# Optimization experiments

Hardware: AMD Instinct MI355X
Metric: run time of the kernel (lower is better)

Reference implementation:

```python
import jax, jax.numpy as jnp
import numpy as np

B, N, D = 4, 1024, 1024
H, DH = 16, 64
N_LAYERS = 3  # len(mlp_dims) - 1 with implicit_mlp_hiddens=(64, 64)
EPS = 1.1920929e-07  # torch.nn.RMSNorm default eps = finfo(float32).eps


def _rope_tables(n, dtype):
    # lucidrains RotaryEmbedding: theta=10000, interleaved freq repeat
    inv_freq = 1.0 / (10000.0 ** (np.arange(0, DH, 2, dtype=np.float64) / DH))
    t = np.arange(n, dtype=np.float64)[:, None] * inv_freq[None, :]  # [n, DH/2]
    t = np.repeat(t, 2, axis=-1)  # [n, DH], freqs interleaved (f0,f0,f1,f1,...)
    return jnp.asarray(np.cos(t), dtype), jnp.asarray(np.sin(t), dtype)


def _rope_rotate(x, cos, sin):
    # x: [b,h,n,d]; rotate_half on interleaved pairs: (x1,x2) -> (-x2,x1)
    xp = x.reshape(*x.shape[:-1], DH // 2, 2)
    xr = jnp.stack((-xp[..., 1], xp[..., 0]), axis=-1).reshape(x.shape)
    return x * cos + xr * sin


def _attend(q, k, v):
    # rotate_queries_with_cached_keys with no cache: same positions for q and k
    n = q.shape[-2]
    cos, sin = _rope_tables(n, q.dtype)
    q = _rope_rotate(q, cos, sin)
    k = _rope_rotate(k, cos, sin)
    scale = DH ** -0.5
    scores = jnp.einsum('bhqd,bhkd->bhqk', q, k) * scale
    causal = jnp.tril(jnp.ones((n, n), dtype=bool))
    scores = jnp.where(causal, scores, -jnp.inf)
    attn = jax.nn.softmax(scores, axis=-1)
    return jnp.einsum('bhqk,bhkd->bhqd', attn, v)


def _split_heads(x):
    b, n, _ = x.shape
    return x.reshape(b, n, H, DH).transpose(0, 2, 1, 3)  # b h n d


def setup_inputs() -> dict:
    key = jax.random.key(0)
    ks = jax.random.split(key, 6)
    s = 0.02
    return {
        'tokens': jax.random.normal(ks[0], (B, N, D), jnp.float32),
        'gamma': jnp.ones((D,), jnp.float32),                                  # RMSNorm weight
        'Wq': jax.random.normal(ks[1], (D, H * DH), jnp.float32) * s,           # to_queries
        'Wk': jax.random.normal(ks[2], (N_LAYERS, D, H * DH), jnp.float32) * s, # stacked key projections
        'Wv': jax.random.normal(ks[3], (N_LAYERS, D, H * DH), jnp.float32) * s, # stacked value projections
        'Wo': jax.random.normal(ks[4], (H * DH, D), jnp.float32) * s,           # to_out
    }


def reference(tokens, gamma, Wq, Wk, Wv, Wo):
    b, n, d = tokens.shape
    # RMSNorm (prenorm)
    x = tokens * jax.lax.rsqrt(jnp.mean(tokens * tokens, axis=-1, keepdims=True) + EPS) * gamma
    out = _split_heads(x @ Wq)  # queries, [b h n d]
    for i in range(N_LAYERS):
        k = _split_heads(x @ Wk[i])
        v = _split_heads(x @ Wv[i])
        out = _attend(out, k, v)
        if i < N_LAYERS - 1:
            out = jax.nn.silu(out)  # implicit MLP activation between attention stages
    out = out.transpose(0, 2, 1, 3).reshape(b, n, H * DH)  # merge heads
    return out @ Wo
```

## Files before the change

### kernel.cpp

```cpp
#include <hip/hip_runtime.h>


typedef unsigned short u16;
typedef short s16x8 __attribute__((ext_vector_type(8)));
typedef u16 u16x4 __attribute__((ext_vector_type(4)));
typedef float f32x4 __attribute__((ext_vector_type(4)));

typedef __attribute__((address_space(1))) const unsigned int as1c_uint;
typedef __attribute__((address_space(3))) unsigned int as3_uint;

__device__ __forceinline__ float b2f(u16 h) {
  union { unsigned int u; float f; } v; v.u = ((unsigned int)h) << 16; return v.f;
}
__device__ __forceinline__ u16 f2b(float f) {
  union { float f; unsigned int u; } v; v.f = f;
  return (u16)((v.u + 0x7FFFu + ((v.u >> 16) & 1u)) >> 16);
}
__device__ __forceinline__ void gload16(const u16* g, const u16* lds) {
  __builtin_amdgcn_global_load_lds((as1c_uint*)(size_t)g,
                                   (as3_uint*)(unsigned int)(size_t)lds, 16, 0, 0);
}

__global__ __launch_bounds__(256)
void rmsnorm_kernel(const float* __restrict__ T, const float* __restrict__ gamma,
                    u16* __restrict__ X) {
  const int row = blockIdx.x, tid = threadIdx.x;
  const float4 v = ((const float4*)(T + (size_t)row * 1024))[tid];
  float ss = v.x * v.x + v.y * v.y + v.z * v.z + v.w * v.w;
#pragma unroll
  for (int msk = 1; msk <= 32; msk <<= 1) ss += __shfl_xor(ss, msk, 64);
  __shared__ float red[4];
  if ((tid & 63) == 0) red[tid >> 6] = ss;
  __syncthreads();
  const float tot = red[0] + red[1] + red[2] + red[3];
  const float r = rsqrtf(tot * (1.0f / 1024.0f) + 1.1920929e-07f);
  const float4 gm = ((const float4*)gamma)[tid];
  u16x4 o;
  o[0] = f2b(v.x * r * gm.x); o[1] = f2b(v.y * r * gm.y);
  o[2] = f2b(v.z * r * gm.z); o[3] = f2b(v.w * r * gm.w);
  *(u16x4*)(X + (size_t)row * 1024 + tid * 4) = o;
}

__global__ __launch_bounds__(256)
void rope_kernel(float* __restrict__ ct, float* __restrict__ st) {
  const int idx = blockIdx.x * 256 + threadIdx.x;
  const int n = idx >> 5, j = idx & 31;
  const double freq = pow(10000.0, -(double)j / 32.0);
  const double a = (double)n * freq;
  ct[idx] = (float)cos(a);
  st[idx] = (float)sin(a);
}

__global__ __launch_bounds__(256)
void transw_kernel(const float* __restrict__ Wq, const float* __restrict__ Wk,
                   const float* __restrict__ Wv, const float* __restrict__ Wo,
                   u16* __restrict__ wt) {
  __shared__ float tile[64][65];
  const int z = blockIdx.z;
  const float* src = (z == 0) ? Wq
                   : (z <= 3) ? (Wk + (size_t)(z - 1) * 1048576)
                   : (z <= 6) ? (Wv + (size_t)(z - 4) * 1048576)
                              : Wo;
  u16* dst = wt + (size_t)z * 1048576;
  const int tid = threadIdx.x;
  const int bx = blockIdx.x * 64;
  const int by = blockIdx.y * 64;
  const int tcol = (tid & 15) * 4, trow = tid >> 4;
#pragma unroll
  for (int i = 0; i < 4; ++i) {
    const int r = trow + i * 16;
    const float4 v = *(const float4*)(src + (size_t)(bx + r) * 1024 + by + tcol);
    tile[r][tcol] = v.x; tile[r][tcol + 1] = v.y;
    tile[r][tcol + 2] = v.z; tile[r][tcol + 3] = v.w;
  }
  __syncthreads();
  const int k4 = (tid & 15) * 4;
#pragma unroll
  for (int j = 0; j < 4; ++j) {
    const int R = (tid >> 4) + j * 16;
    u16x4 o;
    o[0] = f2b(tile[k4][R]);     o[1] = f2b(tile[k4 + 1][R]);
    o[2] = f2b(tile[k4 + 2][R]); o[3] = f2b(tile[k4 + 3][R]);
    *(u16x4*)&dst[(size_t)(by + R) * 1024 + bx + k4] = o;
  }
}

template <int KIND>
__global__ __launch_bounds__(256, 2)
void gemm_kernel(const u16* __restrict__ A, const u16* __restrict__ Bt,
                 void* __restrict__ Cout, const float* __restrict__ ct,
                 const float* __restrict__ st) {
  constexpr int MB = (KIND == 0) ? 8 : 4;
  constexpr int BM = MB * 32;
  constexpr int ASLOT = BM * 32;
  constexpr int SLOT = (BM + 128) * 32;
  const int p = blockIdx.x;
  const int role = (p & 7) * (KIND == 0 ? 112 : 64) + (p >> 3);
  const int z = (KIND == 0) ? (role >> 7) : (role >> 8);
  const int rem = (KIND == 0) ? (role & 127) : (role & 255);
  const int m0 = (rem >> 3) * BM;
  const int n0 = (rem & 7) * 128;

  const int tid = threadIdx.x;
  const int w = tid >> 6, l = tid & 63;
  const int g = l >> 4, ll = l & 15;
  const int wr = w >> 1, wc = w & 1;

  const u16* Ab;
  const u16* Bb;
  if (KIND == 0) {
    Ab = A + (size_t)m0 * 1024;
    Bb = Bt + (size_t)z * 1048576 + (size_t)n0 * 1024;
  } else {
    Ab = A + (size_t)m0 * 1024 + z * 512;
    Bb = Bt + (size_t)n0 * 1024 + z * 512;
  }

  __shared__ u16 SH[3][SLOT];

  const f32x4 zero = {0.f, 0.f, 0.f, 0.f};
  f32x4 acc[MB][4];
#pragma unroll
  for (int i = 0; i < MB; ++i)
#pragma unroll
    for (int j = 0; j < 4; ++j) acc[i][j] = zero;

  auto stage = [&](int t2) {
    const int slot = t2 % 3;
    const int k0 = t2 * 32;
    const int rsub = l >> 2, sl = l & 3;
#pragma unroll
    for (int c = 0; c < MB / 2; ++c) {
      const int chunk = c * 4 + w;
      const int row = chunk * 16 + rsub;
      const int kk = k0 + ((sl ^ ((row >> 1) & 3)) << 3);
      gload16(Ab + (size_t)row * 1024 + kk, &SH[slot][chunk * 512]);
    }
#pragma unroll
    for (int c = 0; c < 2; ++c) {
      const int chunk = c * 4 + w;
      const int row = chunk * 16 + rsub;
      const int kk = k0 + ((sl ^ ((row >> 1) & 3)) << 3);
      gload16(Bb + (size_t)row * 1024 + kk, &SH[slot][ASLOT + chunk * 512]);
    }
  };

  const int NT = (KIND == 1) ? 16 : 32;
  stage(0); stage(1);

#pragma unroll
  for (int t = 0; t < NT; ++t) {
    if (t < NT - 1) {
      if constexpr (KIND == 0) asm volatile("s_waitcnt vmcnt(6)" ::: "memory");
      else                     asm volatile("s_waitcnt vmcnt(4)" ::: "memory");
    } else {
      asm volatile("s_waitcnt vmcnt(0)" ::: "memory");
    }
    __builtin_amdgcn_s_barrier();

    const int slot = t % 3;
    const u16* As = &SH[slot][0];
    const u16* Bs = &SH[slot][ASLOT];
    s16x8 bfr[4];
#pragma unroll
    for (int nf = 0; nf < 4; ++nf) {
      const int row = wc * 64 + nf * 16 + ll;
      bfr[nf] = *(const s16x8*)&Bs[row * 32 + ((g ^ ((row >> 1) & 3)) << 3)];
    }
    s16x8 af[MB];
#pragma unroll
    for (int mf = 0; mf < MB; ++mf) {
      const int row = wr * (MB * 16) + mf * 16 + ll;
      af[mf] = *(const s16x8*)&As[row * 32 + ((g ^ ((row >> 1) & 3)) << 3)];
    }

    if (t + 2 < NT) stage(t + 2);

    __builtin_amdgcn_s_setprio(1);
#pragma unroll
    for (int mf = 0; mf < MB; ++mf)
#pragma unroll
      for (int nf = 0; nf < 4; ++nf)
        acc[mf][nf] = __builtin_amdgcn_mfma_f32_16x16x32_bf16(af[mf], bfr[nf],
                                                              acc[mf][nf], 0, 0, 0);
    __builtin_amdgcn_s_setprio(0);
  }
  __syncthreads();

  if (KIND == 0) {
    u16* C = (u16*)Cout + (size_t)z * 4194304;
    if (z < 4) {
      const bool doRope = (z >= 1);
      u16* T = &SH[0][0];
#pragma unroll
      for (int mf = 0; mf < MB; ++mf)
#pragma unroll
        for (int nf = 0; nf < 4; ++nf) {
          const int c = wc * 64 + nf * 16 + ll;
#pragma unroll
          for (int rg = 0; rg < 4; ++rg) {
            const int r = wr * (MB * 16) + mf * 16 + g * 4 + rg;
            T[r * 128 + (c ^ ((r & 7) << 4))] = f2b(acc[mf][nf][rg]);
          }
        }
      __syncthreads();
#pragma unroll
      for (int i = 0; i < BM / 16; ++i) {
        const int R = (tid >> 4) + i * 16;
        const int c0 = (tid & 15) * 8;
        s16x8 v = *(const s16x8*)&T[R * 128 + (c0 ^ ((R & 7) << 4))];
        if (doRope) {
          const int n = (m0 + R) & 1023;
          const int j0 = (c0 & 63) >> 1;
          const float4 c4 = *(const float4*)(ct + n * 32 + j0);
          const float4 s4 = *(const float4*)(st + n * 32 + j0);
          s16x8 vo;
#pragma unroll
          for (int pp = 0; pp < 4; ++pp) {
            const float c = ((const float*)&c4)[pp];
            const float s = ((const float*)&s4)[pp];
            const float x0 = b2f((u16)v[2 * pp]), x1 = b2f((u16)v[2 * pp + 1]);
            vo[2 * pp]     = (short)f2b(x0 * c - x1 * s);
            vo[2 * pp + 1] = (short)f2b(x1 * c + x0 * s);
          }
          v = vo;
        }
        *(s16x8*)&C[(size_t)(m0 + R) * 1024 + n0 + c0] = v;
      }
    } else {
#pragma unroll
      for (int mf = 0; mf < MB; ++mf)
#pragma unroll
        for (int nf = 0; nf < 4; ++nf) {
          const int col = n0 + wc * 64 + nf * 16 + ll;
          const int hh = col >> 6, d = col & 63;
          const int mb = m0 + wr * (MB * 16) + mf * 16 + g * 4;
          const int bb = mb >> 10, n = mb & 1023;
          u16x4 pk;
#pragma unroll
          for (int rg = 0; rg < 4; ++rg) pk[rg] = f2b(acc[mf][nf][rg]);
          *(u16x4*)&C[((size_t)((bb * 16 + hh) * 64 + d)) * 1024 + n] = pk;
        }
    }
  } else {
    float* C = (float*)Cout + (size_t)z * 4194304;
#pragma unroll
    for (int mf = 0; mf < MB; ++mf)
#pragma unroll
      for (int nf = 0; nf < 4; ++nf) {
        const int col = n0 + wc * 64 + nf * 16 + ll;
#pragma unroll
        for (int rg = 0; rg < 4; ++rg) {
          const int m = m0 + wr * (MB * 16) + mf * 16 + g * 4 + rg;
          C[(size_t)m * 1024 + col] = acc[mf][nf][rg];
        }
      }
  }
}

__global__ __launch_bounds__(256)
void reduce_kernel(const float* __restrict__ P, float* __restrict__ out) {
  const int i = (blockIdx.x * 256 + threadIdx.x) * 4;
  const float4 a = *(const float4*)(P + i);
  const float4 b = *(const float4*)(P + 4194304 + i);
  float4 o;
  o.x = a.x + b.x; o.y = a.y + b.y; o.z = a.z + b.z; o.w = a.w + b.w;
  *(float4*)(out + i) = o;
}

template <int SILU>
__global__ __launch_bounds__(256)
void attn_kernel(const u16* __restrict__ Q, const u16* __restrict__ K,
                 const u16* __restrict__ Vt, u16* __restrict__ O,
                 const float* __restrict__ ct, const float* __restrict__ st) {
  const int lin = blockIdx.x + (blockIdx.y << 3);
  const int role = (lin & 7) * 64 + (lin >> 3);
  const int p = role & 7, bh = role >> 3;
  const int q_lo = p, q_hi = 15 - p;
  const int b = bh >> 4, h = bh & 15;
  const int tid = threadIdx.x, w = tid >> 6, l = tid & 63;
  const int g = l >> 4, ll = l & 15;

  const u16* Qb = Q + (size_t)(b * 1024) * 1024 + h * 64;
  const u16* Kb = K + (size_t)(b * 1024) * 1024 + h * 64;
  const u16* Vb = Vt + (size_t)((b * 16 + h) * 64) * 1024;
  u16* Ob = O + (size_t)(b * 1024) * 1024 + h * 64;

  __shared__ u16 Ksh[2][128 * 72];
  __shared__ u16 Psh[4][16 * 72];

  s16x8 qfL[2], qfH[2];
  auto loadQ = [&](int qt, s16x8* qf) {
    const int qrow = qt * 64 + w * 16 + ll;
#pragma unroll
    for (int kc = 0; kc < 2; ++kc) {
      const int d0 = kc * 32 + g * 8;
      const int j0 = d0 >> 1;
      const float4 c4 = *(const float4*)(ct + qrow * 32 + j0);
      const float4 s4v = *(const float4*)(st + qrow * 32 + j0);
      const s16x8 qin = *(const s16x8*)(Qb + (size_t)qrow * 1024 + d0);
      s16x8 qo;
#pragma unroll
      for (int pp = 0; pp < 4; ++pp) {
        const float c = ((const float*)&c4)[pp], s = ((const float*)&s4v)[pp];
        const float x0 = b2f((u16)qin[2 * pp]), x1 = b2f((u16)qin[2 * pp + 1]);
        qo[2 * pp]     = (short)f2b((x0 * c - x1 * s) * 0.125f);
        qo[2 * pp + 1] = (short)f2b((x1 * c + x0 * s) * 0.125f);
      }
      qf[kc] = qo;
    }
  };
  loadQ(q_lo, qfL);
  loadQ(q_hi, qfH);

  float lsL[4], lsH[4];
  f32x4 oL[4], oH[4];
  const f32x4 zero = {0.f, 0.f, 0.f, 0.f};
#pragma unroll
  for (int rg = 0; rg < 4; ++rg) { lsL[rg] = 0.f; lsH[rg] = 0.f; }
#pragma unroll
  for (int df = 0; df < 4; ++df) { oL[df] = zero; oH[df] = zero; }

  const int srow = tid >> 2;
  const int sc0 = (tid & 3) * 16;

  s16x8 kr0, kr1, kr2, kr3;
  auto kload = [&](int tt) {
    const u16* kp = Kb + (size_t)(tt * 128 + srow) * 1024 + sc0;
    kr0 = *(const s16x8*)kp;
    kr1 = *(const s16x8*)(kp + 8);
    const u16* kp2 = kp + (size_t)64 * 1024;
    kr2 = *(const s16x8*)kp2;
    kr3 = *(const s16x8*)(kp2 + 8);
  };
  auto kstore = [&](int bf) {
    *(s16x8*)&Ksh[bf][srow * 72 + sc0] = kr0;
    *(s16x8*)&Ksh[bf][srow * 72 + sc0 + 8] = kr1;
    *(s16x8*)&Ksh[bf][(64 + srow) * 72 + sc0] = kr2;
    *(s16x8*)&Ksh[bf][(64 + srow) * 72 + sc0 + 8] = kr3;
  };

  kload(0);
  kstore(0);
  __syncthreads();
  int buf = 0;

  const int iters = (q_hi + 2) >> 1;
  for (int tt = 0; tt < iters; ++tt) {
    const bool pre = (tt + 1 < iters);
    if (pre) kload(tt + 1);

    s16x8 vb[2][2][4];
#pragma unroll
    for (int sub = 0; sub < 2; ++sub)
#pragma unroll
      for (int kc = 0; kc < 2; ++kc)
#pragma unroll
        for (int df = 0; df < 4; ++df)
          vb[sub][kc][df] = *(const s16x8*)(Vb + (size_t)(df * 16 + ll) * 1024 +
                                           (tt * 2 + sub) * 64 + kc * 32 + g * 8);

    auto process = [&](const s16x8* qf, float* ls, f32x4* o, int sub,
                       bool diag) {
      const int rb = sub * 64;
      f32x4 s4[4];
      __builtin_amdgcn_s_setprio(1);
#pragma unroll
      for (int nf = 0; nf < 4; ++nf) {
        const s16x8 kb0 = *(const s16x8*)&Ksh[buf][(rb + nf * 16 + ll) * 72 + g * 8];
        const s16x8 kb1 = *(const s16x8*)&Ksh[buf][(rb + nf * 16 + ll) * 72 + 32 + g * 8];
        f32x4 sv = zero;
        sv = __builtin_amdgcn_mfma_f32_16x16x32_bf16(qf[0], kb0, sv, 0, 0, 0);
        sv = __builtin_amdgcn_mfma_f32_16x16x32_bf16(qf[1], kb1, sv, 0, 0, 0);
        s4[nf] = sv;
      }
      __builtin_amdgcn_s_setprio(0);

      if (diag) {
#pragma unroll
        for (int nf = 0; nf < 4; ++nf)
#pragma unroll
          for (int rg = 0; rg < 4; ++rg)
            if (nf * 16 + ll > w * 16 + g * 4 + rg) s4[nf][rg] = -3.0e38f;
      }

#pragma unroll
      for (int rg = 0; rg < 4; ++rg) {
        float ps = 0.f;
#pragma unroll
        for (int nf = 0; nf < 4; ++nf) {
          const float pv = __expf(s4[nf][rg] - 12.f);
          s4[nf][rg] = pv;
          ps += pv;
        }
        ls[rg] += ps;
      }

#pragma unroll
      for (int nf = 0; nf < 4; ++nf)
#pragma unroll
        for (int rg = 0; rg < 4; ++rg)
          Psh[w][(g * 4 + rg) * 72 + nf * 16 + ll] = f2b(s4[nf][rg]);

      __builtin_amdgcn_s_setprio(1);
#pragma unroll
      for (int kc = 0; kc < 2; ++kc) {
        const s16x8 pa = *(const s16x8*)&Psh[w][ll * 72 + kc * 32 + g * 8];
#pragma unroll
        for (int df = 0; df < 4; ++df)
          o[df] = __builtin_amdgcn_mfma_f32_16x16x32_bf16(pa, vb[sub][kc][df],
                                                          o[df], 0, 0, 0);
      }
      __builtin_amdgcn_s_setprio(0);
    };

    const int ka = 2 * tt, kb = 2 * tt + 1;
    process(qfH, lsH, oH, 0, ka == q_hi);
    if (kb <= q_hi) process(qfH, lsH, oH, 1, kb == q_hi);
    if (ka <= q_lo) process(qfL, lsL, oL, 0, ka == q_lo);
    if (kb <= q_lo) process(qfL, lsL, oL, 1, kb == q_lo);

    if (pre) kstore(buf ^ 1);
    __syncthreads();
    buf ^= 1;
  }

  auto finish = [&](float* ls, f32x4* o, int qt) {
#pragma unroll
    for (int rg = 0; rg < 4; ++rg) {
      float v = ls[rg];
      v += __shfl_xor(v, 1, 64);
      v += __shfl_xor(v, 2, 64);
      v += __shfl_xor(v, 4, 64);
      v += __shfl_xor(v, 8, 64);
      ls[rg] = 1.f / v;
    }
#pragma unroll
    for (int df = 0; df < 4; ++df)
#pragma unroll
      for (int rg = 0; rg < 4; ++rg) {
        float val = o[df][rg] * ls[rg];
        if (SILU) val = val / (1.f + __expf(-val));
        Ob[(size_t)(qt * 64 + w * 16 + g * 4 + rg) * 1024 + df * 16 + ll] =
            f2b(val);
      }
  };
  finish(lsH, oH, q_hi);
  finish(lsL, oL, q_lo);
}

extern "C" void kernel_launch(void* const* d_in, const int* in_sizes, int n_in,
                              void* d_out, int out_size, void* d_ws, size_t ws_size,
                              hipStream_t stream) {
  (void)in_sizes; (void)n_in; (void)out_size; (void)ws_size;
  const float* tokens = (const float*)d_in[0];
  const float* gamma  = (const float*)d_in[1];
  const float* Wq     = (const float*)d_in[2];
  const float* Wk     = (const float*)d_in[3];
  const float* Wv     = (const float*)d_in[4];
  const float* Wo     = (const float*)d_in[5];
  float* out = (float*)d_out;

  u16* x    = (u16*)d_ws;
  u16* wt   = x + (size_t)4096 * 1024;
  u16* qkv  = wt + (size_t)8 * 1048576;
  u16* outA = qkv + (size_t)7 * 4194304;
  u16* outB = outA + 4194304;
  float* ct = (float*)(outB + 4194304);
  float* st = ct + 32768;
  float* Pp = (float*)(qkv + 1 * 4194304);

  rmsnorm_kernel<<<4096, 256, 0, stream>>>(tokens, gamma, x);
  rope_kernel<<<128, 256, 0, stream>>>(ct, st);
  transw_kernel<<<dim3(16, 16, 8), 256, 0, stream>>>(Wq, Wk, Wv, Wo, wt);
  gemm_kernel<0><<<896, 256, 0, stream>>>(x, wt, qkv, ct, st);

  const size_t M4 = 4194304;
  attn_kernel<1><<<dim3(8, 64), 256, 0, stream>>>(qkv, qkv + 1 * M4, qkv + 4 * M4,
                                                  outA, ct, st);
  attn_kernel<1><<<dim3(8, 64), 256, 0, stream>>>(outA, qkv + 2 * M4, qkv + 5 * M4,
                                                  outB, ct, st);
  attn_kernel<0><<<dim3(8, 64), 256, 0, stream>>>(outB, qkv + 3 * M4, qkv + 6 * M4,
                                                  outA, ct, st);

  gemm_kernel<1><<<512, 256, 0, stream>>>(outA, wt + (size_t)7 * 1048576,
                                          (void*)Pp, ct, st);
  reduce_kernel<<<4096, 256, 0, stream>>>(Pp, out);
}
```

Measured before the change: 228.8 us.

## Load K fragments directly from global memory instead of staging through LDS

Removes the double-buffered shared-memory K tile and the per-iteration block barrier. Each wave now loads its own K MFMA fragments straight from global memory per 64-key tile, and the loop steps one 64-key tile at a time instead of two. This drops LDS traffic and __syncthreads, but all four waves now fetch the same K data redundantly through cache and lose the register prefetch overlap.

```diff
diff --git a/kernel.cpp b/kernel.cpp
--- a/kernel.cpp
+++ b/kernel.cpp
@@ -286,7 +286,6 @@
   const u16* Vb = Vt + (size_t)((b * 16 + h) * 64) * 1024;
   u16* Ob = O + (size_t)(b * 1024) * 1024 + h * 64;
 
-  __shared__ u16 Ksh[2][128 * 72];
   __shared__ u16 Psh[4][16 * 72];
 
   s16x8 qfL[2], qfH[2];
@@ -321,57 +320,30 @@
 #pragma unroll
   for (int df = 0; df < 4; ++df) { oL[df] = zero; oH[df] = zero; }
 
-  const int srow = tid >> 2;
-  const int sc0 = (tid & 3) * 16;
-
-  s16x8 kr0, kr1, kr2, kr3;
-  auto kload = [&](int tt) {
-    const u16* kp = Kb + (size_t)(tt * 128 + srow) * 1024 + sc0;
-    kr0 = *(const s16x8*)kp;
-    kr1 = *(const s16x8*)(kp + 8);
-    const u16* kp2 = kp + (size_t)64 * 1024;
-    kr2 = *(const s16x8*)kp2;
-    kr3 = *(const s16x8*)(kp2 + 8);
-  };
-  auto kstore = [&](int bf) {
-    *(s16x8*)&Ksh[bf][srow * 72 + sc0] = kr0;
-    *(s16x8*)&Ksh[bf][srow * 72 + sc0 + 8] = kr1;
-    *(s16x8*)&Ksh[bf][(64 + srow) * 72 + sc0] = kr2;
-    *(s16x8*)&Ksh[bf][(64 + srow) * 72 + sc0 + 8] = kr3;
-  };
-
-  kload(0);
-  kstore(0);
-  __syncthreads();
-  int buf = 0;
-
-  const int iters = (q_hi + 2) >> 1;
-  for (int tt = 0; tt < iters; ++tt) {
-    const bool pre = (tt + 1 < iters);
-    if (pre) kload(tt + 1);
-
-    s16x8 vb[2][2][4];
-#pragma unroll
-    for (int sub = 0; sub < 2; ++sub)
-#pragma unroll
-      for (int kc = 0; kc < 2; ++kc)
-#pragma unroll
-        for (int df = 0; df < 4; ++df)
-          vb[sub][kc][df] = *(const s16x8*)(Vb + (size_t)(df * 16 + ll) * 1024 +
-                                           (tt * 2 + sub) * 64 + kc * 32 + g * 8);
-
-    auto process = [&](const s16x8* qf, float* ls, f32x4* o, int sub,
-                       bool diag) {
-      const int rb = sub * 64;
+  for (int t = 0; t <= q_hi; ++t) {
+    s16x8 kf[4][2];
+#pragma unroll
+    for (int nf = 0; nf < 4; ++nf) {
+      const u16* kp = Kb + (size_t)(t * 64 + nf * 16 + ll) * 1024 + g * 8;
+      kf[nf][0] = *(const s16x8*)kp;
+      kf[nf][1] = *(const s16x8*)(kp + 32);
+    }
+    s16x8 vb[2][4];
+#pragma unroll
+    for (int kc = 0; kc < 2; ++kc)
+#pragma unroll
+      for (int df = 0; df < 4; ++df)
+        vb[kc][df] = *(const s16x8*)(Vb + (size_t)(df * 16 + ll) * 1024 +
+                                     t * 64 + kc * 32 + g * 8);
+
+    auto process = [&](const s16x8* qf, float* ls, f32x4* o, bool diag) {
       f32x4 s4[4];
       __builtin_amdgcn_s_setprio(1);
 #pragma unroll
       for (int nf = 0; nf < 4; ++nf) {
-        const s16x8 kb0 = *(const s16x8*)&Ksh[buf][(rb + nf * 16 + ll) * 72 + g * 8];
-        const s16x8 kb1 = *(const s16x8*)&Ksh[buf][(rb + nf * 16 + ll) * 72 + 32 + g * 8];
         f32x4 sv = zero;
-        sv = __builtin_amdgcn_mfma_f32_16x16x32_bf16(qf[0], kb0, sv, 0, 0, 0);
-        sv = __builtin_amdgcn_mfma_f32_16x16x32_bf16(qf[1], kb1, sv, 0, 0, 0);
+        sv = __builtin_amdgcn_mfma_f32_16x16x32_bf16(qf[0], kf[nf][0], sv, 0, 0, 0);
+        sv = __builtin_amdgcn_mfma_f32_16x16x32_bf16(qf[1], kf[nf][1], sv, 0, 0, 0);
         s4[nf] = sv;
       }
       __builtin_amdgcn_s_setprio(0);
@@ -408,21 +380,14 @@
         const s16x8 pa = *(const s16x8*)&Psh[w][ll * 72 + kc * 32 + g * 8];
 #pragma unroll
         for (int df = 0; df < 4; ++df)
-          o[df] = __builtin_amdgcn_mfma_f32_16x16x32_bf16(pa, vb[sub][kc][df],
+          o[df] = __builtin_amdgcn_mfma_f32_16x16x32_bf16(pa, vb[kc][df],
                                                           o[df], 0, 0, 0);
       }
       __builtin_amdgcn_s_setprio(0);
     };
 
-    const int ka = 2 * tt, kb = 2 * tt + 1;
-    process(qfH, lsH, oH, 0, ka == q_hi);
-    if (kb <= q_hi) process(qfH, lsH, oH, 1, kb == q_hi);
-    if (ka <= q_lo) process(qfL, lsL, oL, 0, ka == q_lo);
-    if (kb <= q_lo) process(qfL, lsL, oL, 1, kb == q_lo);
-
-    if (pre) kstore(buf ^ 1);
-    __syncthreads();
-    buf ^= 1;
+    process(qfH, lsH, oH, t == q_hi);
+    if (t <= q_lo) process(qfL, lsL, oL, t == q_lo);
   }
 
   auto finish = [&](float* ls, f32x4* o, int qt) {
```

Result: slower. 301.3 us (+31.7%).

## Fuse three chained attention stages into one kernel keeping queries on-chip

Applied to the files above, without the earlier changes.

Merges the three attention launches into a single kernel that loops over the three layers. Each block keeps its output in registers, applies SiLU and RoPE through shared memory, and reuses the result as the next layer's queries. This removes two kernel launches and the global round trips for the intermediate outputs. The trade-off is more register pressure and an extra barrier per layer. Correctness depends on each block's query tiles only needing its own previous outputs, which holds because the same block handles the same rows in every layer.

```diff
diff --git a/kernel.cpp b/kernel.cpp
--- a/kernel.cpp
+++ b/kernel.cpp
@@ -268,11 +268,10 @@
   *(float4*)(out + i) = o;
 }
 
-template <int SILU>
 __global__ __launch_bounds__(256)
-void attn_kernel(const u16* __restrict__ Q, const u16* __restrict__ K,
-                 const u16* __restrict__ Vt, u16* __restrict__ O,
-                 const float* __restrict__ ct, const float* __restrict__ st) {
+void attn_fused_kernel(const u16* __restrict__ qkv, u16* __restrict__ O,
+                       const float* __restrict__ ct, const float* __restrict__ st) {
+  const size_t M4 = 4194304;
   const int lin = blockIdx.x + (blockIdx.y << 3);
   const int role = (lin & 7) * 64 + (lin >> 3);
   const int p = role & 7, bh = role >> 3;
@@ -281,9 +280,7 @@
   const int tid = threadIdx.x, w = tid >> 6, l = tid & 63;
   const int g = l >> 4, ll = l & 15;
 
-  const u16* Qb = Q + (size_t)(b * 1024) * 1024 + h * 64;
-  const u16* Kb = K + (size_t)(b * 1024) * 1024 + h * 64;
-  const u16* Vb = Vt + (size_t)((b * 16 + h) * 64) * 1024;
+  const u16* Qb = qkv + (size_t)(b * 1024) * 1024 + h * 64;
   u16* Ob = O + (size_t)(b * 1024) * 1024 + h * 64;
 
   __shared__ u16 Ksh[2][128 * 72];
@@ -313,140 +310,188 @@
   loadQ(q_lo, qfL);
   loadQ(q_hi, qfH);
 
+  const f32x4 zero = {0.f, 0.f, 0.f, 0.f};
   float lsL[4], lsH[4];
   f32x4 oL[4], oH[4];
-  const f32x4 zero = {0.f, 0.f, 0.f, 0.f};
-#pragma unroll
-  for (int rg = 0; rg < 4; ++rg) { lsL[rg] = 0.f; lsH[rg] = 0.f; }
-#pragma unroll
-  for (int df = 0; df < 4; ++df) { oL[df] = zero; oH[df] = zero; }
 
   const int srow = tid >> 2;
   const int sc0 = (tid & 3) * 16;
 
-  s16x8 kr0, kr1, kr2, kr3;
-  auto kload = [&](int tt) {
-    const u16* kp = Kb + (size_t)(tt * 128 + srow) * 1024 + sc0;
-    kr0 = *(const s16x8*)kp;
-    kr1 = *(const s16x8*)(kp + 8);
-    const u16* kp2 = kp + (size_t)64 * 1024;
-    kr2 = *(const s16x8*)kp2;
-    kr3 = *(const s16x8*)(kp2 + 8);
-  };
-  auto kstore = [&](int bf) {
-    *(s16x8*)&Ksh[bf][srow * 72 + sc0] = kr0;
-    *(s16x8*)&Ksh[bf][srow * 72 + sc0 + 8] = kr1;
-    *(s16x8*)&Ksh[bf][(64 + srow) * 72 + sc0] = kr2;
-    *(s16x8*)&Ksh[bf][(64 + srow) * 72 + sc0 + 8] = kr3;
-  };
-
-  kload(0);
-  kstore(0);
-  __syncthreads();
-  int buf = 0;
-
-  const int iters = (q_hi + 2) >> 1;
-  for (int tt = 0; tt < iters; ++tt) {
-    const bool pre = (tt + 1 < iters);
-    if (pre) kload(tt + 1);
-
-    s16x8 vb[2][2][4];
-#pragma unroll
-    for (int sub = 0; sub < 2; ++sub)
-#pragma unroll
-      for (int kc = 0; kc < 2; ++kc)
+  for (int layer = 0; layer < 3; ++layer) {
+    const u16* Kb = qkv + (size_t)(1 + layer) * M4 + (size_t)(b * 1024) * 1024 + h * 64;
+    const u16* Vb = qkv + (size_t)(4 + layer) * M4 + (size_t)((b * 16 + h) * 64) * 1024;
+
+#pragma unroll
+    for (int rg = 0; rg < 4; ++rg) { lsL[rg] = 0.f; lsH[rg] = 0.f; }
+#pragma unroll
+    for (int df = 0; df < 4; ++df) { oL[df] = zero; oH[df] = zero; }
+
+    s16x8 kr0, kr1, kr2, kr3;
+    auto kload = [&](int tt) {
+      const u16* kp = Kb + (size_t)(tt * 128 + srow) * 1024 + sc0;
+      kr0 = *(const s16x8*)kp;
+      kr1 = *(const s16x8*)(kp + 8);
+      const u16* kp2 = kp + (size_t)64 * 1024;
+      kr2 = *(const s16x8*)kp2;
+      kr3 = *(const s16x8*)(kp2 + 8);
+    };
+    auto kstore = [&](int bf) {
+      *(s16x8*)&Ksh[bf][srow * 72 + sc0] = kr0;
+      *(s16x8*)&Ksh[bf][srow * 72 + sc0 + 8] = kr1;
+      *(s16x8*)&Ksh[bf][(64 + srow) * 72 + sc0] = kr2;
+      *(s16x8*)&Ksh[bf][(64 + srow) * 72 + sc0 + 8] = kr3;
+    };
+
+    kload(0);
+    kstore(0);
+    __syncthreads();
+    int buf = 0;
+
+    const int iters = (q_hi + 2) >> 1;
+    for (int tt = 0; tt < iters; ++tt) {
+      const bool pre = (tt + 1 < iters);
+      if (pre) kload(tt + 1);
+
+      s16x8 vb[2][2][4];
+#pragma unroll
+      for (int sub = 0; sub < 2; ++sub)
+#pragma unroll
+        for (int kc = 0; kc < 2; ++kc)
+#pragma unroll
+          for (int df = 0; df < 4; ++df)
+            vb[sub][kc][df] = *(const s16x8*)(Vb + (size_t)(df * 16 + ll) * 1024 +
+                                             (tt * 2 + sub) * 64 + kc * 32 + g * 8);
+
+      auto process = [&](const s16x8* qf, float* ls, f32x4* o, int sub,
+                         bool diag) {
+        const int rb = sub * 64;
+        f32x4 s4[4];
+        __builtin_amdgcn_s_setprio(1);
+#pragma unroll
+        for (int nf = 0; nf < 4; ++nf) {
+          const s16x8 kb0 = *(const s16x8*)&Ksh[buf][(rb + nf * 16 + ll) * 72 + g * 8];
+          const s16x8 kb1 = *(const s16x8*)&Ksh[buf][(rb + nf * 16 + ll) * 72 + 32 + g * 8];
+          f32x4 sv = zero;
+          sv = __builtin_amdgcn_mfma_f32_16x16x32_bf16(qf[0], kb0, sv, 0, 0, 0);
+          sv = __builtin_amdgcn_mfma_f32_16x16x32_bf16(qf[1], kb1, sv, 0, 0, 0);
+          s4[nf] = sv;
+        }
+        __builtin_amdgcn_s_setprio(0);
+
+        if (diag) {
+#pragma unroll
+          for (int nf = 0; nf < 4; ++nf)
+#pragma unroll
+            for (int rg = 0; rg < 4; ++rg)
+              if (nf * 16 + ll > w * 16 + g * 4 + rg) s4[nf][rg] = -3.0e38f;
+        }
+
+#pragma unroll
+        for (int rg = 0; rg < 4; ++rg) {
+          float ps = 0.f;
+#pragma unroll
+          for (int nf = 0; nf < 4; ++nf) {
+            const float pv = __expf(s4[nf][rg] - 12.f);
+            s4[nf][rg] = pv;
+            ps += pv;
+          }
+          ls[rg] += ps;
+        }
+
+#pragma unroll
+        for (int nf = 0; nf < 4; ++nf)
+#pragma unroll
+          for (int rg = 0; rg < 4; ++rg)
+            Psh[w][(g * 4 + rg) * 72 + nf * 16 + ll] = f2b(s4[nf][rg]);
+
+        __builtin_amdgcn_s_setprio(1);
+#pragma unroll
+        for (int kc = 0; kc < 2; ++kc) {
+          const s16x8 pa = *(const s16x8*)&Psh[w][ll * 72 + kc * 32 + g * 8];
+#pragma unroll
+          for (int df = 0; df < 4; ++df)
+            o[df] = __builtin_amdgcn_mfma_f32_16x16x32_bf16(pa, vb[sub][kc][df],
+                                                            o[df], 0, 0, 0);
+        }
+        __builtin_amdgcn_s_setprio(0);
+      };
+
+      const int ka = 2 * tt, kb2 = 2 * tt + 1;
+      process(qfH, lsH, oH, 0, ka == q_hi);
+      if (kb2 <= q_hi) process(qfH, lsH, oH, 1, kb2 == q_hi);
+      if (ka <= q_lo) process(qfL, lsL, oL, 0, ka == q_lo);
+      if (kb2 <= q_lo) process(qfL, lsL, oL, 1, kb2 == q_lo);
+
+      if (pre) kstore(buf ^ 1);
+      __syncthreads();
+      buf ^= 1;
+    }
+
+    if (layer < 2) {
+      auto toQ = [&](float* ls, f32x4* o, int qt, s16x8* qf) {
+#pragma unroll
+        for (int rg = 0; rg < 4; ++rg) {
+          float v = ls[rg];
+          v += __shfl_xor(v, 1, 64);
+          v += __shfl_xor(v, 2, 64);
+          v += __shfl_xor(v, 4, 64);
+          v += __shfl_xor(v, 8, 64);
+          ls[rg] = 1.f / v;
+        }
 #pragma unroll
         for (int df = 0; df < 4; ++df)
-          vb[sub][kc][df] = *(const s16x8*)(Vb + (size_t)(df * 16 + ll) * 1024 +
-                                           (tt * 2 + sub) * 64 + kc * 32 + g * 8);
-
-    auto process = [&](const s16x8* qf, float* ls, f32x4* o, int sub,
-                       bool diag) {
-      const int rb = sub * 64;
-      f32x4 s4[4];
-      __builtin_amdgcn_s_setprio(1);
-#pragma unroll
-      for (int nf = 0; nf < 4; ++nf) {
-        const s16x8 kb0 = *(const s16x8*)&Ksh[buf][(rb + nf * 16 + ll) * 72 + g * 8];
-        const s16x8 kb1 = *(const s16x8*)&Ksh[buf][(rb + nf * 16 + ll) * 72 + 32 + g * 8];
-        f32x4 sv = zero;
-        sv = __builtin_amdgcn_mfma_f32_16x16x32_bf16(qf[0], kb0, sv, 0, 0, 0);
-        sv = __builtin_amdgcn_mfma_f32_16x16x32_bf16(qf[1], kb1, sv, 0, 0, 0);
-        s4[nf] = sv;
-      }
-      __builtin_amdgcn_s_setprio(0);
-
-      if (diag) {
-#pragma unroll
-        for (int nf = 0; nf < 4; ++nf)
-#pragma unroll
-          for (int rg = 0; rg < 4; ++rg)
-            if (nf * 16 + ll > w * 16 + g * 4 + rg) s4[nf][rg] = -3.0e38f;
-      }
-
-#pragma unroll
-      for (int rg = 0; rg < 4; ++rg) {
-        float ps = 0.f;
-#pragma unroll
-        for (int nf = 0; nf < 4; ++nf) {
-          const float pv = __expf(s4[nf][rg] - 12.f);
-          s4[nf][rg] = pv;
-          ps += pv;
-        }
-        ls[rg] += ps;
-      }
-
-#pragma unroll
-      for (int nf = 0; nf < 4; ++nf)
-#pragma unroll
-        for (int rg = 0; rg < 4; ++rg)
-          Psh[w][(g * 4 + rg) * 72 + nf * 16 + ll] = f2b(s4[nf][rg]);
-
-      __builtin_amdgcn_s_setprio(1);
-#pragma unroll
-      for (int kc = 0; kc < 2; ++kc) {
-        const s16x8 pa = *(const s16x8*)&Psh[w][ll * 72 + kc * 32 + g * 8];
+#pragma unroll
+          for (int rg = 0; rg < 4; ++rg) {
+            float val = o[df][rg] * ls[rg];
+            val = val / (1.f + __expf(-val));
+            Psh[w][(g * 4 + rg) * 72 + df * 16 + ll] = f2b(val);
+          }
+        const int qrow = qt * 64 + w * 16 + ll;
+#pragma unroll
+        for (int kc = 0; kc < 2; ++kc) {
+          const int d0 = kc * 32 + g * 8;
+          const int j0 = d0 >> 1;
+          const float4 c4 = *(const float4*)(ct + qrow * 32 + j0);
+          const float4 s4v = *(const float4*)(st + qrow * 32 + j0);
+          const s16x8 qin = *(const s16x8*)&Psh[w][ll * 72 + d0];
+          s16x8 qo;
+#pragma unroll
+          for (int pp = 0; pp < 4; ++pp) {
+            const float c = ((const float*)&c4)[pp], s = ((const float*)&s4v)[pp];
+            const float x0 = b2f((u16)qin[2 * pp]), x1 = b2f((u16)qin[2 * pp + 1]);
+            qo[2 * pp]     = (short)f2b((x0 * c - x1 * s) * 0.125f);
+            qo[2 * pp + 1] = (short)f2b((x1 * c + x0 * s) * 0.125f);
+          }
+          qf[kc] = qo;
+        }
+      };
+      toQ(lsH, oH, q_hi, qfH);
+      toQ(lsL, oL, q_lo, qfL);
+      __syncthreads();
+    } else {
+      auto finish = [&](float* ls, f32x4* o, int qt) {
+#pragma unroll
+        for (int rg = 0; rg < 4; ++rg) {
+          float v = ls[rg];
+          v += __shfl_xor(v, 1, 64);
+          v += __shfl_xor(v, 2, 64);
+          v += __shfl_xor(v, 4, 64);
+          v += __shfl_xor(v, 8, 64);
+          ls[rg] = 1.f / v;
+        }
 #pragma unroll
         for (int df = 0; df < 4; ++df)
-          o[df] = __builtin_amdgcn_mfma_f32_16x16x32_bf16(pa, vb[sub][kc][df],
-                                                          o[df], 0, 0, 0);
-      }
-      __builtin_amdgcn_s_setprio(0);
-    };
-
-    const int ka = 2 * tt, kb = 2 * tt + 1;
-    process(qfH, lsH, oH, 0, ka == q_hi);
-    if (kb <= q_hi) process(qfH, lsH, oH, 1, kb == q_hi);
-    if (ka <= q_lo) process(qfL, lsL, oL, 0, ka == q_lo);
-    if (kb <= q_lo) process(qfL, lsL, oL, 1, kb == q_lo);
-
-    if (pre) kstore(buf ^ 1);
-    __syncthreads();
-    buf ^= 1;
+#pragma unroll
+          for (int rg = 0; rg < 4; ++rg) {
+            const float val = o[df][rg] * ls[rg];
+            Ob[(size_t)(qt * 64 + w * 16 + g * 4 + rg) * 1024 + df * 16 + ll] =
+                f2b(val);
+          }
+      };
+      finish(lsH, oH, q_hi);
+      finish(lsL, oL, q_lo);
+    }
   }
-
-  auto finish = [&](float* ls, f32x4* o, int qt) {
-#pragma unroll
-    for (int rg = 0; rg < 4; ++rg) {
-      float v = ls[rg];
-      v += __shfl_xor(v, 1, 64);
-      v += __shfl_xor(v, 2, 64);
-      v += __shfl_xor(v, 4, 64);
-      v += __shfl_xor(v, 8, 64);
-      ls[rg] = 1.f / v;
-    }
-#pragma unroll
-    for (int df = 0; df < 4; ++df)
-#pragma unroll
-      for (int rg = 0; rg < 4; ++rg) {
-        float val = o[df][rg] * ls[rg];
-        if (SILU) val = val / (1.f + __expf(-val));
-        Ob[(size_t)(qt * 64 + w * 16 + g * 4 + rg) * 1024 + df * 16 + ll] =
-            f2b(val);
-      }
-  };
-  finish(lsH, oH, q_hi);
-  finish(lsL, oL, q_lo);
 }
 
 extern "C" void kernel_launch(void* const* d_in, const int* in_sizes, int n_in,
@@ -475,13 +520,7 @@
   transw_kernel<<<dim3(16, 16, 8), 256, 0, stream>>>(Wq, Wk, Wv, Wo, wt);
   gemm_kernel<0><<<896, 256, 0, stream>>>(x, wt, qkv, ct, st);
 
-  const size_t M4 = 4194304;
-  attn_kernel<1><<<dim3(8, 64), 256, 0, stream>>>(qkv, qkv + 1 * M4, qkv + 4 * M4,
-                                                  outA, ct, st);
-  attn_kernel<1><<<dim3(8, 64), 256, 0, stream>>>(outA, qkv + 2 * M4, qkv + 5 * M4,
-                                                  outB, ct, st);
-  attn_kernel<0><<<dim3(8, 64), 256, 0, stream>>>(outB, qkv + 3 * M4, qkv + 6 * M4,
-                                                  outA, ct, st);
+  attn_fused_kernel<<<dim3(8, 64), 256, 0, stream>>>(qkv, outA, ct, st);
 
   gemm_kernel<1><<<512, 256, 0, stream>>>(outA, wt + (size_t)7 * 1048576,
                                           (void*)Pp, ct, st);
```

Result: slower. 242.0 us (+5.8%).
